# Performance work log

Hardware: AMD Instinct MI355X
Metric: run time of the kernel (lower is better)

## Reference

```python
import jax, jax.numpy as jnp
import numpy as np

N_NODES = 100000
IN_C = 512
HID = 64   # 2 * out_channels
OUT_C = 32
N_EDGES = 2000000  # knn k=20


def gcn_conv(x, src, dst, W, b, n_nodes):
    """PyG GCNConv: symmetric norm with self-loops. Aggregates src -> dst."""
    h = x @ W  # [N, F_out] -- transform first (F_out small)
    ones = jnp.ones(src.shape[0], dtype=h.dtype)
    deg = jax.ops.segment_sum(ones, dst, num_segments=n_nodes) + 1.0  # +1 self-loop
    dinv = jax.lax.rsqrt(deg)  # deg > 0 always due to self-loop
    norm = dinv[src] * dinv[dst]                      # [E]
    msg = h[src] * norm[:, None]                      # gather + scale
    agg = jax.ops.segment_sum(msg, dst, num_segments=n_nodes)
    agg = agg + (dinv * dinv)[:, None] * h            # self-loop contribution
    return agg + b


def setup_inputs() -> dict:
    key = jax.random.key(0)
    ks = jax.random.split(key, 9)
    x = jax.random.normal(ks[0], (N_NODES, IN_C), dtype=jnp.float32)
    edge_index = jax.random.randint(ks[1], (2, N_EDGES), 0, N_NODES, dtype=jnp.int64)
    s1 = 1.0 / np.sqrt(IN_C)
    s2 = 1.0 / np.sqrt(HID)
    W1 = jax.random.uniform(ks[2], (IN_C, HID), jnp.float32, -s1, s1)
    b1 = jnp.zeros((HID,), jnp.float32)
    W_mu = jax.random.uniform(ks[3], (HID, OUT_C), jnp.float32, -s2, s2)
    b_mu = jnp.zeros((OUT_C,), jnp.float32)
    W_ls = jax.random.uniform(ks[4], (HID, OUT_C), jnp.float32, -s2, s2)
    b_ls = jnp.zeros((OUT_C,), jnp.float32)
    return {"x": x, "edge_index": edge_index, "W1": W1, "b1": b1,
            "W_mu": W_mu, "b_mu": b_mu, "W_ls": W_ls, "b_ls": b_ls}


def reference(x, edge_index, W1, b1, W_mu, b_mu, W_ls, b_ls):
    src, dst = edge_index[0], edge_index[1]  # source_to_target flow
    h = jax.nn.relu(gcn_conv(x, src, dst, W1, b1, N_NODES))
    mu = gcn_conv(h, src, dst, W_mu, b_mu, N_NODES)
    logstd = gcn_conv(h, src, dst, W_ls, b_ls, N_NODES)
    return (mu, logstd)
```

## Files before the change

kernel.cpp:

```cpp
#include <hip/hip_runtime.h>
#include <cstdint>
#include <cstddef>

#define MN 100000
#define NE 2000000
#define BSH 7
#define BKN 128
#define NB  782
#define CAP 3072
#define EPB 8192

typedef short bf16x8 __attribute__((ext_vector_type(8)));
typedef float f32x4  __attribute__((ext_vector_type(4)));
typedef unsigned short u16x8 __attribute__((ext_vector_type(8)));

__device__ inline unsigned short f2bf(float f) {
    unsigned int u = __float_as_uint(f);
    unsigned int r = (u + 0x7fffu + ((u >> 16) & 1u)) >> 16;
    return (unsigned short)r;
}
__device__ inline float bf2f(unsigned short h) {
    return __uint_as_float((unsigned int)h << 16);
}
__device__ inline float rdlane(float v, int l) {
    return __uint_as_float((unsigned int)__builtin_amdgcn_readlane((int)__float_as_uint(v), l));
}

__global__ __launch_bounds__(256) void w1_convert(const float* __restrict__ W,
                                                  unsigned short* __restrict__ Whi,
                                                  unsigned short* __restrict__ Wlo,
                                                  int* __restrict__ gcur) {
    const int t = blockIdx.x * 256 + threadIdx.x;
    if (t < NB) gcur[t] = 0;
    const int col = t & 63;
    const int kb  = (t >> 6) * 8;
    union { unsigned short u[8]; int4 v; } hp, lp;
#pragma unroll
    for (int j = 0; j < 8; ++j) {
        float wv = W[(size_t)(kb + j) * 64 + col];
        unsigned short hh = f2bf(wv);
        hp.u[j] = hh;
        lp.u[j] = f2bf(wv - bf2f(hh));
    }
    *reinterpret_cast<int4*>(Whi + (size_t)t * 8) = hp.v;
    *reinterpret_cast<int4*>(Wlo + (size_t)t * 8) = lp.v;
}

__global__ __launch_bounds__(1024) void bin_kernel(const int* __restrict__ src,
                                                   const int* __restrict__ dst,
                                                   int* __restrict__ gcur,
                                                   unsigned int* __restrict__ binned,
                                                   int nE) {
    __shared__ int hist[NB];
    __shared__ int base[NB];
    const int tid = threadIdx.x;
    const int e0 = blockIdx.x * EPB;
    const int e1 = min(e0 + EPB, nE);

    for (int i = tid; i < NB; i += 1024) hist[i] = 0;
    __syncthreads();
    for (int e = e0 + tid * 4; e < e1; e += 4096) {
        if (e + 4 <= e1) {
            int4 d4 = *reinterpret_cast<const int4*>(dst + e);
            atomicAdd(&hist[d4.x >> BSH], 1);
            atomicAdd(&hist[d4.y >> BSH], 1);
            atomicAdd(&hist[d4.z >> BSH], 1);
            atomicAdd(&hist[d4.w >> BSH], 1);
        } else {
            for (int k = e; k < e1; ++k) atomicAdd(&hist[dst[k] >> BSH], 1);
        }
    }
    __syncthreads();
    for (int i = tid; i < NB; i += 1024) {
        int h = hist[i];
        base[i] = (h > 0) ? atomicAdd(&gcur[i], h) : 0;
        hist[i] = 0;
    }
    __syncthreads();
    for (int e = e0 + tid * 4; e < e1; e += 4096) {
        if (e + 4 <= e1) {
            int4 d4 = *reinterpret_cast<const int4*>(dst + e);
            int4 s4 = *reinterpret_cast<const int4*>(src + e);
            int dd[4] = {d4.x, d4.y, d4.z, d4.w};
            int ss[4] = {s4.x, s4.y, s4.z, s4.w};
#pragma unroll
            for (int k = 0; k < 4; ++k) {
                int b = dd[k] >> BSH;
                int p = base[b] + atomicAdd(&hist[b], 1);
                if (p < CAP)
                    binned[(size_t)b * CAP + p] =
                        ((unsigned int)ss[k] << BSH) | (unsigned int)(dd[k] & (BKN - 1));
            }
        } else {
            for (int k = e; k < e1; ++k) {
                int d = dst[k];
                int b = d >> BSH;
                int p = base[b] + atomicAdd(&hist[b], 1);
                if (p < CAP)
                    binned[(size_t)b * CAP + p] =
                        ((unsigned int)src[k] << BSH) | (unsigned int)(d & (BKN - 1));
            }
        }
    }
}

__global__ __launch_bounds__(256) void csr_build(const unsigned int* __restrict__ binned,
                                                 const int* __restrict__ gcur,
                                                 int* __restrict__ rowptr,
                                                 int* __restrict__ rowend,
                                                 float* __restrict__ dinv,
                                                 int* __restrict__ csr, int M) {
    __shared__ int cnt[BKN];
    __shared__ int pre[BKN];
    __shared__ int cur[BKN];
    const int tid = threadIdx.x, b = blockIdx.x;
    const unsigned int* seg = binned + (size_t)b * CAP;
    const int n = min(gcur[b], CAP);

    if (tid < BKN) cnt[tid] = 0;
    __syncthreads();
    for (int i = tid; i < n; i += 256)
        atomicAdd(&cnt[seg[i] & (BKN - 1)], 1);
    __syncthreads();
    if (tid < BKN) pre[tid] = cnt[tid];
    __syncthreads();
#pragma unroll
    for (int off = 1; off < BKN; off <<= 1) {
        int t = 0;
        if (tid < BKN && tid >= off) t = pre[tid - off];
        __syncthreads();
        if (tid < BKN) pre[tid] += t;
        __syncthreads();
    }
    const int node0 = b << BSH;
    if (tid < BKN) {
        int g = b * CAP + pre[tid] - cnt[tid];
        cur[tid] = g;
        int node = node0 + tid;
        if (node < M) {
            rowptr[node] = g;
            rowend[node] = g + cnt[tid];
            dinv[node] = rsqrtf((float)cnt[tid] + 1.0f);
        }
    }
    __syncthreads();
    for (int i = tid; i < n; i += 256) {
        unsigned int pk = seg[i];
        int p = atomicAdd(&cur[pk & (BKN - 1)], 1);
        csr[p] = (int)(pk >> BSH);
    }
}

__global__ __launch_bounds__(256) void gemm1_mfma(const float* __restrict__ x,
                                                  const unsigned short* __restrict__ Whi,
                                                  const unsigned short* __restrict__ Wlo,
                                                  const float* __restrict__ dinv,
                                                  unsigned short* __restrict__ out, int M) {
    const int tid  = threadIdx.x;
    const int lane = tid & 63;
    const int wid  = tid >> 6;
    const int bm   = blockIdx.x * 64;
    const int kg   = lane >> 4;
    const int rlo  = lane & 15;
    const int arow = bm + wid * 16 + rlo;
    const bool rok = arow < M;
    const float* aptr = x + (size_t)arow * 512 + kg * 8;

    f32x4 acc[4];
#pragma unroll
    for (int c = 0; c < 4; ++c)
#pragma unroll
        for (int r = 0; r < 4; ++r) acc[c][r] = 0.f;

    for (int s = 0; s < 16; ++s) {
        float av[8];
        if (rok) {
            float4 p0 = *reinterpret_cast<const float4*>(aptr + s * 32);
            float4 p1 = *reinterpret_cast<const float4*>(aptr + s * 32 + 4);
            av[0] = p0.x; av[1] = p0.y; av[2] = p0.z; av[3] = p0.w;
            av[4] = p1.x; av[5] = p1.y; av[6] = p1.z; av[7] = p1.w;
        } else {
#pragma unroll
            for (int j = 0; j < 8; ++j) av[j] = 0.f;
        }
        union { unsigned short u[8]; bf16x8 v; } ah, al;
#pragma unroll
        for (int j = 0; j < 8; ++j) {
            unsigned short h = f2bf(av[j]);
            ah.u[j] = h;
            al.u[j] = f2bf(av[j] - bf2f(h));
        }
        const size_t cb = ((size_t)((s * 4 + kg) * 64 + rlo)) * 8;
#pragma unroll
        for (int c = 0; c < 4; ++c) {
            bf16x8 bh = *reinterpret_cast<const bf16x8*>(Whi + cb + (size_t)c * 16 * 8);
            bf16x8 bl = *reinterpret_cast<const bf16x8*>(Wlo + cb + (size_t)c * 16 * 8);
            acc[c] = __builtin_amdgcn_mfma_f32_16x16x32_bf16(ah.v, bh, acc[c], 0, 0, 0);
            acc[c] = __builtin_amdgcn_mfma_f32_16x16x32_bf16(al.v, bh, acc[c], 0, 0, 0);
            acc[c] = __builtin_amdgcn_mfma_f32_16x16x32_bf16(ah.v, bl, acc[c], 0, 0, 0);
        }
    }

#pragma unroll
    for (int reg = 0; reg < 4; ++reg) {
        int node = bm + wid * 16 + kg * 4 + reg;
        if (node < M) {
            float di = dinv[node];
#pragma unroll
            for (int c = 0; c < 4; ++c)
                out[(size_t)node * 64 + c * 16 + rlo] = f2bf(acc[c][reg] * di);
        }
    }
}

__global__ __launch_bounds__(256) void agg1_kernel(const unsigned short* __restrict__ hs1,
                                                   const int* __restrict__ rowptr,
                                                   const int* __restrict__ rowend,
                                                   const int* __restrict__ csr,
                                                   const float* __restrict__ dinv,
                                                   const float* __restrict__ b1,
                                                   unsigned short* __restrict__ hs2, int M) {
    const int lane = threadIdx.x & 63;
    const int g = lane >> 3, q = lane & 7;
    const int node = blockIdx.x * 4 + (threadIdx.x >> 6);
    if (node >= M) return;
    const int st = rowptr[node], en = rowend[node];
    const size_t qo = (size_t)q * 8;
    float a[8];
#pragma unroll
    for (int j = 0; j < 8; ++j) a[j] = 0.f;
    int i = st;
    for (; i + 16 <= en; i += 16) {
        int sa = csr[i + g];
        int sb = csr[i + 8 + g];
        u16x8 va = *reinterpret_cast<const u16x8*>(hs1 + (size_t)sa * 64 + qo);
        u16x8 vb = *reinterpret_cast<const u16x8*>(hs1 + (size_t)sb * 64 + qo);
#pragma unroll
        for (int j = 0; j < 8; ++j) a[j] += bf2f(va[j]) + bf2f(vb[j]);
    }
    for (; i < en; i += 8) {
        int e = i + g;
        if (e < en) {
            int s = csr[e];
            u16x8 v = *reinterpret_cast<const u16x8*>(hs1 + (size_t)s * 64 + qo);
#pragma unroll
            for (int j = 0; j < 8; ++j) a[j] += bf2f(v[j]);
        }
    }
#pragma unroll
    for (int m = 8; m <= 32; m <<= 1)
#pragma unroll
        for (int j = 0; j < 8; ++j) a[j] += __shfl_xor(a[j], m);

    if (g == 0) {
        u16x8 sv = *reinterpret_cast<const u16x8*>(hs1 + (size_t)node * 64 + qo);
        float di = dinv[node];
        float4 b0 = *reinterpret_cast<const float4*>(b1 + qo);
        float4 b4 = *reinterpret_cast<const float4*>(b1 + qo + 4);
        float bb[8] = {b0.x, b0.y, b0.z, b0.w, b4.x, b4.y, b4.z, b4.w};
        u16x8 hv;
#pragma unroll
        for (int j = 0; j < 8; ++j)
            hv[j] = f2bf(fmaxf(di * (a[j] + bf2f(sv[j])) + bb[j], 0.f) * di);
        *reinterpret_cast<u16x8*>(hs2 + (size_t)node * 64 + qo) = hv;
    }
}

__global__ __launch_bounds__(256) void agg2_fused(const unsigned short* __restrict__ hs2,
                                                  const int* __restrict__ rowptr,
                                                  const int* __restrict__ rowend,
                                                  const int* __restrict__ csr,
                                                  const float* __restrict__ dinv,
                                                  const float* __restrict__ Wmu,
                                                  const float* __restrict__ bmu,
                                                  const float* __restrict__ Wls,
                                                  const float* __restrict__ bls,
                                                  float* __restrict__ out, int M) {
    __shared__ float Wc[64][64];
    const int tid = threadIdx.x;
    const int lane = tid & 63;
    const int wid = tid >> 6;
    const int g = lane >> 3, q = lane & 7;
    const size_t qo = (size_t)q * 8;

    for (int t = tid; t < 4096; t += 256) {
        int k = t >> 6, c = t & 63;
        Wc[k][c] = (c < 32) ? Wmu[k * 32 + c] : Wls[k * 32 + (c - 32)];
    }
    __syncthreads();

    const float bval = (lane < 32) ? bmu[lane] : bls[lane - 32];
    const int node0 = blockIdx.x * 32;

    for (int rp = 0; rp < 4; ++rp) {
        const int n0 = node0 + wid * 8 + rp * 2;
        const int n1 = n0 + 1;
        if (n0 >= M) break;
        const bool ok1 = n1 < M;

        float a0[8], a1[8];
#pragma unroll
        for (int j = 0; j < 8; ++j) { a0[j] = 0.f; a1[j] = 0.f; }

        {
            const int st = rowptr[n0], en = rowend[n0];
            int i = st;
            for (; i + 16 <= en; i += 16) {
                int sa = csr[i + g];
                int sb = csr[i + 8 + g];
                u16x8 va = *reinterpret_cast<const u16x8*>(hs2 + (size_t)sa * 64 + qo);
                u16x8 vb = *reinterpret_cast<const u16x8*>(hs2 + (size_t)sb * 64 + qo);
#pragma unroll
                for (int j = 0; j < 8; ++j) a0[j] += bf2f(va[j]) + bf2f(vb[j]);
            }
            for (; i < en; i += 8) {
                int e = i + g;
                if (e < en) {
                    int s = csr[e];
                    u16x8 v = *reinterpret_cast<const u16x8*>(hs2 + (size_t)s * 64 + qo);
#pragma unroll
                    for (int j = 0; j < 8; ++j) a0[j] += bf2f(v[j]);
                }
            }
        }
        if (ok1) {
            const int st = rowptr[n1], en = rowend[n1];
            int i = st;
            for (; i + 16 <= en; i += 16) {
                int sa = csr[i + g];
                int sb = csr[i + 8 + g];
                u16x8 va = *reinterpret_cast<const u16x8*>(hs2 + (size_t)sa * 64 + qo);
                u16x8 vb = *reinterpret_cast<const u16x8*>(hs2 + (size_t)sb * 64 + qo);
#pragma unroll
                for (int j = 0; j < 8; ++j) a1[j] += bf2f(va[j]) + bf2f(vb[j]);
            }
            for (; i < en; i += 8) {
                int e = i + g;
                if (e < en) {
                    int s = csr[e];
                    u16x8 v = *reinterpret_cast<const u16x8*>(hs2 + (size_t)s * 64 + qo);
#pragma unroll
                    for (int j = 0; j < 8; ++j) a1[j] += bf2f(v[j]);
                }
            }
        }

#pragma unroll
        for (int m = 8; m <= 32; m <<= 1)
#pragma unroll
            for (int j = 0; j < 8; ++j) {
                a0[j] += __shfl_xor(a0[j], m);
                a1[j] += __shfl_xor(a1[j], m);
            }

        {
            u16x8 sv0 = *reinterpret_cast<const u16x8*>(hs2 + (size_t)n0 * 64 + qo);
            float di0 = dinv[n0];
#pragma unroll
            for (int j = 0; j < 8; ++j) a0[j] = di0 * (a0[j] + bf2f(sv0[j]));
            if (ok1) {
                u16x8 sv1 = *reinterpret_cast<const u16x8*>(hs2 + (size_t)n1 * 64 + qo);
                float di1 = dinv[n1];
#pragma unroll
                for (int j = 0; j < 8; ++j) a1[j] = di1 * (a1[j] + bf2f(sv1[j]));
            }
        }

        float o0 = bval, o1 = bval;
#pragma unroll
        for (int k = 0; k < 64; ++k) {
            float w = Wc[k][lane];
            o0 = fmaf(rdlane(a0[k & 7], k >> 3), w, o0);
            o1 = fmaf(rdlane(a1[k & 7], k >> 3), w, o1);
        }

        if (lane < 32) {
            out[(size_t)n0 * 32 + lane] = o0;
            if (ok1) out[(size_t)n1 * 32 + lane] = o1;
        } else {
            out[(size_t)MN * 32 + (size_t)n0 * 32 + (lane - 32)] = o0;
            if (ok1) out[(size_t)MN * 32 + (size_t)n1 * 32 + (lane - 32)] = o1;
        }
    }
}

extern "C" void kernel_launch(void* const* d_in, const int* in_sizes, int n_in,
                              void* d_out, int out_size, void* d_ws, size_t ws_size,
                              hipStream_t stream) {
    const float* x   = (const float*)d_in[0];
    const int*   ei  = (const int*)d_in[1];
    const float* W1  = (const float*)d_in[2];
    const float* b1  = (const float*)d_in[3];
    const float* Wmu = (const float*)d_in[4];
    const float* bmu = (const float*)d_in[5];
    const float* Wls = (const float*)d_in[6];
    const float* bls = (const float*)d_in[7];
    float* out = (float*)d_out;

    const int M = MN, E = NE;
    const int* src = ei;
    const int* dst = ei + E;

    const size_t bf_feat_bytes = (size_t)M * 64 * sizeof(unsigned short);
    char* w = (char*)d_ws;
    size_t off = 0;
    auto alloc = [&](size_t bytes) {
        char* p = w + off;
        off = (off + bytes + 255) & ~(size_t)255;
        return p;
    };
    int*            gcur   = (int*)           alloc((size_t)NB * 4);
    unsigned int*   binned = (unsigned int*)  alloc((size_t)NB * CAP * 4);
    int*            rowptr = (int*)           alloc((size_t)M * 4);
    int*            rowend = (int*)           alloc((size_t)M * 4);
    int*            csr    = (int*)           alloc((size_t)NB * CAP * 4);
    float*          dinv   = (float*)         alloc((size_t)M * 4);
    unsigned short* Whi    = (unsigned short*)alloc((size_t)512 * 64 * 2);
    unsigned short* Wlo    = (unsigned short*)alloc((size_t)512 * 64 * 2);
    unsigned short* hs1    = (unsigned short*)alloc(bf_feat_bytes);
    unsigned short* hs2    = (unsigned short*)alloc(bf_feat_bytes);

    w1_convert<<<16, 256, 0, stream>>>(W1, Whi, Wlo, gcur);
    bin_kernel<<<(E + EPB - 1) / EPB, 1024, 0, stream>>>(src, dst, gcur, binned, E);
    csr_build<<<NB, 256, 0, stream>>>(binned, gcur, rowptr, rowend, dinv, csr, M);

    gemm1_mfma<<<(M + 63) / 64, 256, 0, stream>>>(x, Whi, Wlo, dinv, hs1, M);
    agg1_kernel<<<(M + 3) / 4, 256, 0, stream>>>(hs1, rowptr, rowend, csr, dinv, b1, hs2, M);
    agg2_fused<<<(M + 31) / 32, 256, 0, stream>>>(hs2, rowptr, rowend, csr, dinv,
                                                  Wmu, bmu, Wls, bls, out, M);
}
```

Before: 222.5 us.

## Halve bin block size, cache CSR segment in registers, 3-way masked gather

```diff
diff --git a/kernel.cpp b/kernel.cpp
--- a/kernel.cpp
+++ b/kernel.cpp
@@ -8,7 +8,7 @@
 #define BKN 128
 #define NB  782
 #define CAP 3072
-#define EPB 8192
+#define EPB 4096
 
 typedef short bf16x8 __attribute__((ext_vector_type(8)));
 typedef float f32x4  __attribute__((ext_vector_type(4)));
@@ -56,19 +56,19 @@
     const int tid = threadIdx.x;
     const int e0 = blockIdx.x * EPB;
     const int e1 = min(e0 + EPB, nE);
+    const int e  = e0 + tid * 4;
+    const bool have = (e + 4 <= e1);
 
     for (int i = tid; i < NB; i += 1024) hist[i] = 0;
     __syncthreads();
-    for (int e = e0 + tid * 4; e < e1; e += 4096) {
-        if (e + 4 <= e1) {
-            int4 d4 = *reinterpret_cast<const int4*>(dst + e);
-            atomicAdd(&hist[d4.x >> BSH], 1);
-            atomicAdd(&hist[d4.y >> BSH], 1);
-            atomicAdd(&hist[d4.z >> BSH], 1);
-            atomicAdd(&hist[d4.w >> BSH], 1);
-        } else {
-            for (int k = e; k < e1; ++k) atomicAdd(&hist[dst[k] >> BSH], 1);
-        }
+
+    int4 d4 = make_int4(0, 0, 0, 0);
+    if (have) {
+        d4 = *reinterpret_cast<const int4*>(dst + e);
+        atomicAdd(&hist[d4.x >> BSH], 1);
+        atomicAdd(&hist[d4.y >> BSH], 1);
+        atomicAdd(&hist[d4.z >> BSH], 1);
+        atomicAdd(&hist[d4.w >> BSH], 1);
     }
     __syncthreads();
     for (int i = tid; i < NB; i += 1024) {
@@ -77,29 +77,17 @@
         hist[i] = 0;
     }
     __syncthreads();
-    for (int e = e0 + tid * 4; e < e1; e += 4096) {
-        if (e + 4 <= e1) {
-            int4 d4 = *reinterpret_cast<const int4*>(dst + e);
-            int4 s4 = *reinterpret_cast<const int4*>(src + e);
-            int dd[4] = {d4.x, d4.y, d4.z, d4.w};
-            int ss[4] = {s4.x, s4.y, s4.z, s4.w};
-#pragma unroll
-            for (int k = 0; k < 4; ++k) {
-                int b = dd[k] >> BSH;
-                int p = base[b] + atomicAdd(&hist[b], 1);
-                if (p < CAP)
-                    binned[(size_t)b * CAP + p] =
-                        ((unsigned int)ss[k] << BSH) | (unsigned int)(dd[k] & (BKN - 1));
-            }
-        } else {
-            for (int k = e; k < e1; ++k) {
-                int d = dst[k];
-                int b = d >> BSH;
-                int p = base[b] + atomicAdd(&hist[b], 1);
-                if (p < CAP)
-                    binned[(size_t)b * CAP + p] =
-                        ((unsigned int)src[k] << BSH) | (unsigned int)(d & (BKN - 1));
-            }
+    if (have) {
+        int4 s4 = *reinterpret_cast<const int4*>(src + e);
+        int dd[4] = {d4.x, d4.y, d4.z, d4.w};
+        int ss[4] = {s4.x, s4.y, s4.z, s4.w};
+#pragma unroll
+        for (int k = 0; k < 4; ++k) {
+            int b = dd[k] >> BSH;
+            int p = base[b] + atomicAdd(&hist[b], 1);
+            if (p < CAP)
+                binned[(size_t)b * CAP + p] =
+                    ((unsigned int)ss[k] << BSH) | (unsigned int)(dd[k] & (BKN - 1));
         }
     }
 }
@@ -119,9 +107,18 @@
 
     if (tid < BKN) cnt[tid] = 0;
     __syncthreads();
-    for (int i = tid; i < n; i += 256)
-        atomicAdd(&cnt[seg[i] & (BKN - 1)], 1);
-    __syncthreads();
+
+    unsigned int mys[12];
+#pragma unroll
+    for (int k = 0; k < 12; ++k) {
+        int i = tid + (k << 8);
+        mys[k] = (i < n) ? seg[i] : 0xFFFFFFFFu;
+    }
+#pragma unroll
+    for (int k = 0; k < 12; ++k)
+        if (mys[k] != 0xFFFFFFFFu) atomicAdd(&cnt[mys[k] & (BKN - 1)], 1);
+    __syncthreads();
+
     if (tid < BKN) pre[tid] = cnt[tid];
     __syncthreads();
 #pragma unroll
@@ -144,11 +141,13 @@
         }
     }
     __syncthreads();
-    for (int i = tid; i < n; i += 256) {
-        unsigned int pk = seg[i];
-        int p = atomicAdd(&cur[pk & (BKN - 1)], 1);
-        csr[p] = (int)(pk >> BSH);
-    }
+#pragma unroll
+    for (int k = 0; k < 12; ++k)
+        if (mys[k] != 0xFFFFFFFFu) {
+            unsigned int pk = mys[k];
+            int p = atomicAdd(&cur[pk & (BKN - 1)], 1);
+            csr[p] = (int)(pk >> BSH);
+        }
 }
 
 __global__ __launch_bounds__(256) void gemm1_mfma(const float* __restrict__ x,
@@ -213,6 +212,27 @@
     }
 }
 
+__device__ inline void gather3(const unsigned short* __restrict__ hs,
+                               const int* __restrict__ csr,
+                               int st, int en, int g, size_t qo, float a[8]) {
+    for (int i = st; i < en; i += 24) {
+        int e0 = i + g, e1 = i + 8 + g, e2 = i + 16 + g;
+        int c0 = (e0 < en) ? e0 : st;
+        int c1 = (e1 < en) ? e1 : st;
+        int c2 = (e2 < en) ? e2 : st;
+        float m0 = (e0 < en) ? 1.f : 0.f;
+        float m1 = (e1 < en) ? 1.f : 0.f;
+        float m2 = (e2 < en) ? 1.f : 0.f;
+        int s0 = csr[c0], s1 = csr[c1], s2 = csr[c2];
+        u16x8 v0 = *reinterpret_cast<const u16x8*>(hs + (size_t)s0 * 64 + qo);
+        u16x8 v1 = *reinterpret_cast<const u16x8*>(hs + (size_t)s1 * 64 + qo);
+        u16x8 v2 = *reinterpret_cast<const u16x8*>(hs + (size_t)s2 * 64 + qo);
+#pragma unroll
+        for (int j = 0; j < 8; ++j)
+            a[j] += m0 * bf2f(v0[j]) + m1 * bf2f(v1[j]) + m2 * bf2f(v2[j]);
+    }
+}
+
 __global__ __launch_bounds__(256) void agg1_kernel(const unsigned short* __restrict__ hs1,
                                                    const int* __restrict__ rowptr,
                                                    const int* __restrict__ rowend,
@@ -229,24 +249,9 @@
     float a[8];
 #pragma unroll
     for (int j = 0; j < 8; ++j) a[j] = 0.f;
-    int i = st;
-    for (; i + 16 <= en; i += 16) {
-        int sa = csr[i + g];
-        int sb = csr[i + 8 + g];
-        u16x8 va = *reinterpret_cast<const u16x8*>(hs1 + (size_t)sa * 64 + qo);
-        u16x8 vb = *reinterpret_cast<const u16x8*>(hs1 + (size_t)sb * 64 + qo);
-#pragma unroll
-        for (int j = 0; j < 8; ++j) a[j] += bf2f(va[j]) + bf2f(vb[j]);
-    }
-    for (; i < en; i += 8) {
-        int e = i + g;
-        if (e < en) {
-            int s = csr[e];
-            u16x8 v = *reinterpret_cast<const u16x8*>(hs1 + (size_t)s * 64 + qo);
-#pragma unroll
-            for (int j = 0; j < 8; ++j) a[j] += bf2f(v[j]);
-        }
-    }
+
+    gather3(hs1, csr, st, en, g, qo, a);
+
 #pragma unroll
     for (int m = 8; m <= 32; m <<= 1)
 #pragma unroll
@@ -302,48 +307,8 @@
 #pragma unroll
         for (int j = 0; j < 8; ++j) { a0[j] = 0.f; a1[j] = 0.f; }
 
-        {
-            const int st = rowptr[n0], en = rowend[n0];
-            int i = st;
-            for (; i + 16 <= en; i += 16) {
-                int sa = csr[i + g];
-                int sb = csr[i + 8 + g];
-                u16x8 va = *reinterpret_cast<const u16x8*>(hs2 + (size_t)sa * 64 + qo);
-                u16x8 vb = *reinterpret_cast<const u16x8*>(hs2 + (size_t)sb * 64 + qo);
-#pragma unroll
-                for (int j = 0; j < 8; ++j) a0[j] += bf2f(va[j]) + bf2f(vb[j]);
-            }
-            for (; i < en; i += 8) {
-                int e = i + g;
-                if (e < en) {
-                    int s = csr[e];
-                    u16x8 v = *reinterpret_cast<const u16x8*>(hs2 + (size_t)s * 64 + qo);
-#pragma unroll
-                    for (int j = 0; j < 8; ++j) a0[j] += bf2f(v[j]);
-                }
-            }
-        }
-        if (ok1) {
-            const int st = rowptr[n1], en = rowend[n1];
-            int i = st;
-            for (; i + 16 <= en; i += 16) {
-                int sa = csr[i + g];
-                int sb = csr[i + 8 + g];
-                u16x8 va = *reinterpret_cast<const u16x8*>(hs2 + (size_t)sa * 64 + qo);
-                u16x8 vb = *reinterpret_cast<const u16x8*>(hs2 + (size_t)sb * 64 + qo);
-#pragma unroll
-                for (int j = 0; j < 8; ++j) a1[j] += bf2f(va[j]) + bf2f(vb[j]);
-            }
-            for (; i < en; i += 8) {
-                int e = i + g;
-                if (e < en) {
-                    int s = csr[e];
-                    u16x8 v = *reinterpret_cast<const u16x8*>(hs2 + (size_t)s * 64 + qo);
-#pragma unroll
-                    for (int j = 0; j < 8; ++j) a1[j] += bf2f(v[j]);
-                }
-            }
-        }
+        gather3(hs2, csr, rowptr[n0], rowend[n0], g, qo, a0);
+        if (ok1) gather3(hs2, csr, rowptr[n1], rowend[n1], g, qo, a1);
 
 #pragma unroll
         for (int m = 8; m <= 32; m <<= 1)
@@ -413,7 +378,7 @@
     unsigned int*   binned = (unsigned int*)  alloc((size_t)NB * CAP * 4);
     int*            rowptr = (int*)           alloc((size_t)M * 4);
     int*            rowend = (int*)           alloc((size_t)M * 4);
-    int*            csr    = (int*)           alloc((size_t)NB * CAP * 4);
+    int*            csr    = (int*)           alloc((size_t)NB * CAP * 4 + 256);
     float*          dinv   = (float*)         alloc((size_t)M * 4);
     unsigned short* Whi    = (unsigned short*)alloc((size_t)512 * 64 * 2);
     unsigned short* Wlo    = (unsigned short*)alloc((size_t)512 * 64 * 2);
```

After: 213.5 us. 4.0% less time.
